# Performance work log

Hardware: AMD Instinct MI355X
Metric: run time of the kernel (lower is better)

The kernel has to match this reference:

```python
import jax, jax.numpy as jnp
import numpy as np

# Segmented linear polynomial: irreps '96x0e + 64x1o + 32x2e' -> same
MULS_IN = (96, 64, 32)   # input multiplicities per irrep segment
MULS_OUT = (96, 64, 32)  # output multiplicities per irrep segment
IRREP_DIMS = (1, 3, 5)   # 2l+1 for l = 0, 1, 2
NUM_ELEMENTS = 64        # number of indexed weight sets
BATCH = 16384            # nodes
IN_SIZE = sum(m * d for m, d in zip(MULS_IN, IRREP_DIMS))    # 448
OUT_SIZE = sum(m * d for m, d in zip(MULS_OUT, IRREP_DIMS))  # 448
W_SIZE = sum(mi * mo for mi, mo in zip(MULS_IN, MULS_OUT))   # 14336


def setup_inputs() -> dict:
    key = jax.random.key(0)
    k1, k2, k3 = jax.random.split(key, 3)
    weights = jax.random.normal(k1, (NUM_ELEMENTS, W_SIZE), dtype=jnp.float32)
    x = jax.random.normal(k2, (BATCH, IN_SIZE), dtype=jnp.float32)
    weight_indices = jax.random.randint(k3, (BATCH,), 0, NUM_ELEMENTS, dtype=jnp.int64)
    return {"weights": weights, "x": x, "weight_indices": weight_indices}


def reference(weights, x, weight_indices):
    """Indexed segmented linear: per irrep segment,
    y[b, o, m] = sum_i x[b, i, m] * W[idx[b], i, o]."""
    B = x.shape[0]
    outs = []
    w_off = 0
    x_off = 0
    for mi, mo, d in zip(MULS_IN, MULS_OUT, IRREP_DIMS):
        W_seg = weights[:, w_off:w_off + mi * mo].reshape(-1, mi, mo)  # [E, mi, mo]
        x_seg = x[:, x_off:x_off + mi * d].reshape(B, mi, d)           # [B, mi, d]
        Wg = W_seg[weight_indices]                                     # [B, mi, mo] gather
        y_seg = jnp.einsum('bim,bio->bom', x_seg, Wg)                  # [B, mo, d]
        outs.append(y_seg.reshape(B, mo * d))
        w_off += mi * mo
        x_off += mi * d
    return jnp.concatenate(outs, axis=1)  # [B, OUT_SIZE]
```

## Files before the change

### kernel.cpp

```cpp
#include <hip/hip_runtime.h>


#define BATCH     16384
#define IN_SIZE   448
#define OUT_SIZE  448
#define W_SIZE    14336
#define NELEM     64
#define RTILE     32
#define MAXTILES  576
#define WT_ELEM   15872

typedef __attribute__((ext_vector_type(8))) short short8;
typedef __attribute__((ext_vector_type(8))) unsigned short us8;
typedef __attribute__((ext_vector_type(4))) float f32x4;

__device__ __forceinline__ unsigned short f2bf(float f) {
    unsigned int u = __float_as_uint(f);
    u += 0x7fffu + ((u >> 16) & 1u);
    return (unsigned short)(u >> 16);
}


template <int MI, int MO, int SRC, int DB>
__device__ __forceinline__ void wprep_seg(const float* __restrict__ we,
                                          unsigned short* __restrict__ de,
                                          unsigned short* lw, int t) {
    constexpr int LP  = MO + 4;
    constexpr int STR = MI + 8;
    constexpr int CNT = MI * MO;
    constexpr int C8  = STR / 8;

    for (int g = t * 4; g < CNT; g += 1024) {
        const int i = g / MO, o = g - i * MO;
        const float4 v = *(const float4*)(we + SRC + g);
        ushort4 w = { f2bf(v.x), f2bf(v.y), f2bf(v.z), f2bf(v.w) };
        *(ushort4*)&lw[i * LP + o] = w;
    }
    __syncthreads();

    for (int c = t; c < MO * C8; c += 256) {
        const int o = c / C8, i0 = (c - o * C8) * 8;
        us8 w;
        #pragma unroll
        for (int k = 0; k < 8; ++k)
            w[k] = (i0 + k < MI) ? lw[(i0 + k) * LP + o] : (unsigned short)0;
        *(us8*)&de[DB + o * STR + i0] = w;
    }
}

__global__ __launch_bounds__(256) void combo_kernel(
    const int* __restrict__ widx, const float* __restrict__ weights,
    int* __restrict__ offsets, int* __restrict__ tileoff, int* __restrict__ blk2e,
    unsigned short* __restrict__ wt) {
    __shared__ __align__(16) unsigned short lw[9600];
    const int t = threadIdx.x;

    if (blockIdx.x < 192) {
        const int e = blockIdx.x / 3, seg = blockIdx.x - 3 * (blockIdx.x / 3);
        const float* __restrict__ we = weights + (size_t)e * W_SIZE;
        unsigned short* __restrict__ de = wt + (size_t)e * WT_ELEM;
        if (seg == 0)      wprep_seg<96, 96,     0,     0>(we, de, lw, t);
        else if (seg == 1) wprep_seg<64, 64,  9216,  9984>(we, de, lw, t);
        else               wprep_seg<32, 32, 13312, 14592>(we, de, lw, t);
        return;
    }

    __shared__ int h[NELEM];
    __shared__ int off_s[NELEM + 1], tl_s[NELEM + 1];
    if (t < NELEM) h[t] = 0;
    __syncthreads();
    for (int i = 0; i < 64; ++i)
        atomicAdd(&h[widx[i * 256 + t]], 1);
    __syncthreads();
    if (t == 0) {
        int o = 0, tl = 0;
        for (int e = 0; e < NELEM; ++e) {
            off_s[e] = o; tl_s[e] = tl;
            o += h[e]; tl += (h[e] + RTILE - 1) >> 5;
        }
        off_s[NELEM] = o; tl_s[NELEM] = tl;
    }
    __syncthreads();
    if (t <= NELEM) { offsets[t] = off_s[t]; tileoff[t] = tl_s[t]; }
    for (int i = t; i < MAXTILES; i += 256) blk2e[i] = -1;
    __syncthreads();
    if (t < NELEM)
        for (int bb = tl_s[t]; bb < tl_s[t + 1]; ++bb) blk2e[bb] = t;
}


template <int MI, int MO, int D, int XOFF, int YOFF, int WB>
__device__ __forceinline__ void do_seg(const float* __restrict__ x,
                                       const unsigned short* __restrict__ wt_e,
                                       const int* rid_s, int nrows,
                                       float* __restrict__ out,
                                       unsigned short* lds_w, unsigned short* lds_x,
                                       int t) {
    constexpr int XP   = MI * D + 8;
    constexpr int WSTR = MI + 8;
    constexpr int NT   = MO / 16;
    constexpr int KB   = MI / 32;
    constexpr int MTL  = 2 * D;
    constexpr int WCH  = (MO * WSTR) / 8;
    constexpr int FPT  = (MI * D) / 8;
    constexpr int NQ   = FPT / 4;
    constexpr int MOD  = MO * D;
    constexpr int NTW  = (MTL * NT) / 4;
    constexpr int F4R  = MOD / 4;

    const int r = t >> 3, j = t & 7;

    const float4* __restrict__ src =
        (const float4*)(x + (size_t)rid_s[r] * IN_SIZE + XOFF + j * FPT);
    float vv[FPT];
    #pragma unroll
    for (int q = 0; q < NQ; ++q) {
        const float4 v = src[q];
        vv[q * 4 + 0] = v.x; vv[q * 4 + 1] = v.y;
        vv[q * 4 + 2] = v.z; vv[q * 4 + 3] = v.w;
    }

    const uint4* __restrict__ wsrc = (const uint4*)(wt_e + WB);
    for (int idx = t; idx < WCH; idx += 256) ((uint4*)lds_w)[idx] = wsrc[idx];

    if (D == 1) {
        #pragma unroll
        for (int q = 0; q < NQ; ++q) {
            ushort4 w = { f2bf(vv[q * 4 + 0]), f2bf(vv[q * 4 + 1]),
                          f2bf(vv[q * 4 + 2]), f2bf(vv[q * 4 + 3]) };
            *(ushort4*)&lds_x[r * XP + j * FPT + q * 4] = w;
        }
    } else if (D == 3) {
        #pragma unroll
        for (int m = 0; m < 3; ++m) {
            us8 w;
            #pragma unroll
            for (int bq = 0; bq < 8; ++bq) w[bq] = f2bf(vv[3 * bq + m]);
            *(us8*)&lds_x[r * XP + m * MI + j * 8] = w;
        }
    } else {
        #pragma unroll
        for (int m = 0; m < 5; ++m) {
            ushort4 w = { f2bf(vv[m]), f2bf(vv[5 + m]),
                          f2bf(vv[10 + m]), f2bf(vv[15 + m]) };
            *(ushort4*)&lds_x[r * XP + m * MI + j * 4] = w;
        }
    }
    __syncthreads();

    const int lane = t & 63, w = t >> 6;
    const int row_l = lane & 15, kg = lane >> 4;
    f32x4 accs[NTW];
    #pragma unroll
    for (int q = 0; q < NTW; ++q) {
        const int ct = w + q * 4;
        const int mIdx = ct / NT, nt = ct - mIdx * NT;
        const int mt = mIdx & 1, mch = mIdx >> 1;
        f32x4 acc = {0.f, 0.f, 0.f, 0.f};
        #pragma unroll
        for (int kb = 0; kb < KB; ++kb) {
            const short8 a = *(const short8*)&lds_x[(mt * 16 + row_l) * XP + mch * MI + kb * 32 + kg * 8];
            const short8 b = *(const short8*)&lds_w[(nt * 16 + row_l) * WSTR + kb * 32 + kg * 8];
            acc = __builtin_amdgcn_mfma_f32_16x16x32_bf16(a, b, acc, 0, 0, 0);
        }
        accs[q] = acc;
    }
    __syncthreads();

    float* __restrict__ lout = (float*)lds_w;
    #pragma unroll
    for (int q = 0; q < NTW; ++q) {
        const int ct = w + q * 4;
        const int mIdx = ct / NT, nt = ct - mIdx * NT;
        const int mt = mIdx & 1, mch = mIdx >> 1;
        const int o = nt * 16 + row_l;
        #pragma unroll
        for (int jj = 0; jj < 4; ++jj) {
            const int m = mt * 16 + kg * 4 + jj;
            lout[m * MOD + o * D + mch] = accs[q][jj];
        }
    }
    __syncthreads();

    for (int idx = t; idx < RTILE * F4R; idx += 256) {
        const int rr = idx / F4R, c = idx - rr * F4R;
        if (rr < nrows) {
            float4 v = *(const float4*)&lout[rr * MOD + c * 4];
            *(float4*)&out[(size_t)rid_s[rr] * OUT_SIZE + YOFF + c * 4] = v;
        }
    }
}

__global__ __launch_bounds__(256) void gemm_kernel(
    const float* __restrict__ x, const unsigned short* __restrict__ wt,
    const int* __restrict__ widx, const int* __restrict__ offsets,
    const int* __restrict__ tileoff, const int* __restrict__ blk2e,
    float* __restrict__ out) {
    __shared__ __align__(16) unsigned short lds[13312];
    __shared__ int rid_s[RTILE];
    __shared__ int wsum[4];

    const int t   = threadIdx.x;
    const int seg = blockIdx.x / MAXTILES;
    const int tb  = blockIdx.x - seg * MAXTILES;
    const int e   = blk2e[tb];
    if (e < 0) return;
    const int tile  = tb - tileoff[e];
    const int cnt   = offsets[e + 1] - offsets[e];
    const int lo    = tile * RTILE;
    const int nrows = min(RTILE, cnt - lo);

    {
        unsigned long long m = 0;
        #pragma unroll
        for (int i = 0; i < 64; ++i)
            m |= (unsigned long long)(widx[i * 256 + t] == e) << i;
        const int c = __popcll(m);
        int xacc = c;
        #pragma unroll
        for (int d = 1; d < 64; d <<= 1) {
            const int v = __shfl_up(xacc, d, 64);
            if ((t & 63) >= d) xacc += v;
        }
        if ((t & 63) == 63) wsum[t >> 6] = xacc;
        __syncthreads();
        int wbase = 0;
        #pragma unroll
        for (int wv = 0; wv < 4; ++wv) wbase += (wv < (t >> 6)) ? wsum[wv] : 0;
        const int p = wbase + xacc - c;
        if (p < lo + RTILE && p + c > lo) {
            unsigned long long mm = m;
            int k = p;
            while (mm) {
                const int i = __ffsll((long long)mm) - 1;
                if (k >= lo) rid_s[k - lo] = i * 256 + t;
                ++k;
                if (k >= lo + RTILE) break;
                mm &= mm - 1;
            }
        }
        __syncthreads();
        if (t >= nrows && t < RTILE) rid_s[t] = rid_s[0];
        __syncthreads();
    }

    const unsigned short* wt_e = wt + (size_t)e * WT_ELEM;
    if (seg == 0)
        do_seg<96, 96, 1,   0,   0,     0>(x, wt_e, rid_s, nrows, out, lds, lds + 9984, t);
    else if (seg == 1)
        do_seg<64, 64, 3,  96,  96,  9984>(x, wt_e, rid_s, nrows, out, lds, lds + 4608, t);
    else
        do_seg<32, 32, 5, 288, 288, 14592>(x, wt_e, rid_s, nrows, out, lds, lds + 1280, t);
}


extern "C" void kernel_launch(void* const* d_in, const int* in_sizes, int n_in,
                              void* d_out, int out_size, void* d_ws, size_t ws_size,
                              hipStream_t stream) {
    const float* weights = (const float*)d_in[0];
    const float* x       = (const float*)d_in[1];
    const int*   widx    = (const int*)d_in[2];
    float*       out     = (float*)d_out;

    char* ws = (char*)d_ws;
    int* offsets = (int*)(ws + 0);
    int* tileoff = (int*)(ws + 512);
    int* blk2e   = (int*)(ws + 1024);
    unsigned short* wt = (unsigned short*)(ws + 8192);

    combo_kernel<<<193, 256, 0, stream>>>(widx, weights, offsets, tileoff, blk2e, wt);
    gemm_kernel <<<3 * MAXTILES, 256, 0, stream>>>(x, wt, widx, offsets,
                                                   tileoff, blk2e, out);
}
```

Before: 31.48 us.

## Double row tile to 64, prefetch weights early, use contiguous index scan

Raises the rows per tile from 32 to 64, so each block reuses the staged per-element weight slice across twice as many rows and fewer blocks are launched. Each thread now loads two rows of x, each wave computes twice as many MFMA tiles, and the output is written through LDS in two 32-row passes. The weight copy into LDS is moved ahead of the row-id scan so it overlaps with that scan. The index scan now reads contiguous 64-entry chunks per thread instead of strided entries. This costs more registers and LDS per block and leaves fewer blocks to spread across CUs, and partially filled 64-row tiles waste more compute.

```diff
diff --git a/kernel.cpp b/kernel.cpp
--- a/kernel.cpp
+++ b/kernel.cpp
@@ -6,8 +6,8 @@
 #define OUT_SIZE  448
 #define W_SIZE    14336
 #define NELEM     64
-#define RTILE     32
-#define MAXTILES  576
+#define RTILE     64
+#define MAXTILES  320
 #define WT_ELEM   15872
 
 typedef __attribute__((ext_vector_type(8))) short short8;
@@ -76,7 +76,7 @@
         int o = 0, tl = 0;
         for (int e = 0; e < NELEM; ++e) {
             off_s[e] = o; tl_s[e] = tl;
-            o += h[e]; tl += (h[e] + RTILE - 1) >> 5;
+            o += h[e]; tl += (h[e] + RTILE - 1) >> 6;
         }
         off_s[NELEM] = o; tl_s[NELEM] = tl;
     }
@@ -89,61 +89,65 @@
 }
 
 
-template <int MI, int MO, int D, int XOFF, int YOFF, int WB>
+template <int MI, int MO, int D, int XOFF, int YOFF, int WB, int WHALVES>
 __device__ __forceinline__ void do_seg(const float* __restrict__ x,
                                        const unsigned short* __restrict__ wt_e,
                                        const int* rid_s, int nrows,
                                        float* __restrict__ out,
-                                       unsigned short* lds_w, unsigned short* lds_x,
-                                       int t) {
+                                       unsigned short* lds, int t) {
     constexpr int XP   = MI * D + 8;
     constexpr int WSTR = MI + 8;
     constexpr int NT   = MO / 16;
     constexpr int KB   = MI / 32;
-    constexpr int MTL  = 2 * D;
-    constexpr int WCH  = (MO * WSTR) / 8;
     constexpr int FPT  = (MI * D) / 8;
     constexpr int NQ   = FPT / 4;
     constexpr int MOD  = MO * D;
-    constexpr int NTW  = (MTL * NT) / 4;
+    constexpr int NTW  = D * NT;
     constexpr int F4R  = MOD / 4;
 
+    unsigned short* lds_w = lds;
+    unsigned short* lds_x = lds + WHALVES;
+
     const int r = t >> 3, j = t & 7;
 
-    const float4* __restrict__ src =
-        (const float4*)(x + (size_t)rid_s[r] * IN_SIZE + XOFF + j * FPT);
-    float vv[FPT];
-    #pragma unroll
-    for (int q = 0; q < NQ; ++q) {
-        const float4 v = src[q];
-        vv[q * 4 + 0] = v.x; vv[q * 4 + 1] = v.y;
-        vv[q * 4 + 2] = v.z; vv[q * 4 + 3] = v.w;
-    }
-
-    const uint4* __restrict__ wsrc = (const uint4*)(wt_e + WB);
-    for (int idx = t; idx < WCH; idx += 256) ((uint4*)lds_w)[idx] = wsrc[idx];
-
-    if (D == 1) {
+    float vv[2][FPT];
+    #pragma unroll
+    for (int rr = 0; rr < 2; ++rr) {
+        const float4* __restrict__ src =
+            (const float4*)(x + (size_t)rid_s[r + rr * 32] * IN_SIZE + XOFF + j * FPT);
         #pragma unroll
         for (int q = 0; q < NQ; ++q) {
-            ushort4 w = { f2bf(vv[q * 4 + 0]), f2bf(vv[q * 4 + 1]),
-                          f2bf(vv[q * 4 + 2]), f2bf(vv[q * 4 + 3]) };
-            *(ushort4*)&lds_x[r * XP + j * FPT + q * 4] = w;
-        }
-    } else if (D == 3) {
-        #pragma unroll
-        for (int m = 0; m < 3; ++m) {
-            us8 w;
+            const float4 v = src[q];
+            vv[rr][q * 4 + 0] = v.x; vv[rr][q * 4 + 1] = v.y;
+            vv[rr][q * 4 + 2] = v.z; vv[rr][q * 4 + 3] = v.w;
+        }
+    }
+
+    #pragma unroll
+    for (int rr = 0; rr < 2; ++rr) {
+        unsigned short* __restrict__ dst = lds_x + (r + rr * 32) * XP;
+        if (D == 1) {
             #pragma unroll
-            for (int bq = 0; bq < 8; ++bq) w[bq] = f2bf(vv[3 * bq + m]);
-            *(us8*)&lds_x[r * XP + m * MI + j * 8] = w;
-        }
-    } else {
-        #pragma unroll
-        for (int m = 0; m < 5; ++m) {
-            ushort4 w = { f2bf(vv[m]), f2bf(vv[5 + m]),
-                          f2bf(vv[10 + m]), f2bf(vv[15 + m]) };
-            *(ushort4*)&lds_x[r * XP + m * MI + j * 4] = w;
+            for (int q = 0; q < NQ; ++q) {
+                ushort4 w = { f2bf(vv[rr][q * 4 + 0]), f2bf(vv[rr][q * 4 + 1]),
+                              f2bf(vv[rr][q * 4 + 2]), f2bf(vv[rr][q * 4 + 3]) };
+                *(ushort4*)&dst[j * FPT + q * 4] = w;
+            }
+        } else if (D == 3) {
+            #pragma unroll
+            for (int m = 0; m < 3; ++m) {
+                us8 w;
+                #pragma unroll
+                for (int bq = 0; bq < 8; ++bq) w[bq] = f2bf(vv[rr][3 * bq + m]);
+                *(us8*)&dst[m * MI + j * 8] = w;
+            }
+        } else {
+            #pragma unroll
+            for (int m = 0; m < 5; ++m) {
+                ushort4 w = { f2bf(vv[rr][m]), f2bf(vv[rr][5 + m]),
+                              f2bf(vv[rr][10 + m]), f2bf(vv[rr][15 + m]) };
+                *(ushort4*)&dst[m * MI + j * 4] = w;
+            }
         }
     }
     __syncthreads();
@@ -155,7 +159,7 @@
     for (int q = 0; q < NTW; ++q) {
         const int ct = w + q * 4;
         const int mIdx = ct / NT, nt = ct - mIdx * NT;
-        const int mt = mIdx & 1, mch = mIdx >> 1;
+        const int mt = mIdx & 3, mch = mIdx >> 2;
         f32x4 acc = {0.f, 0.f, 0.f, 0.f};
         #pragma unroll
         for (int kb = 0; kb < KB; ++kb) {
@@ -167,27 +171,33 @@
     }
     __syncthreads();
 
-    float* __restrict__ lout = (float*)lds_w;
-    #pragma unroll
-    for (int q = 0; q < NTW; ++q) {
-        const int ct = w + q * 4;
-        const int mIdx = ct / NT, nt = ct - mIdx * NT;
-        const int mt = mIdx & 1, mch = mIdx >> 1;
-        const int o = nt * 16 + row_l;
-        #pragma unroll
-        for (int jj = 0; jj < 4; ++jj) {
-            const int m = mt * 16 + kg * 4 + jj;
-            lout[m * MOD + o * D + mch] = accs[q][jj];
-        }
-    }
-    __syncthreads();
-
-    for (int idx = t; idx < RTILE * F4R; idx += 256) {
-        const int rr = idx / F4R, c = idx - rr * F4R;
-        if (rr < nrows) {
-            float4 v = *(const float4*)&lout[rr * MOD + c * 4];
-            *(float4*)&out[(size_t)rid_s[rr] * OUT_SIZE + YOFF + c * 4] = v;
-        }
+    float* __restrict__ lout = (float*)lds;
+    #pragma unroll
+    for (int p = 0; p < 2; ++p) {
+        #pragma unroll
+        for (int q = 0; q < NTW; ++q) {
+            const int ct = w + q * 4;
+            const int mIdx = ct / NT, nt = ct - mIdx * NT;
+            const int mt = mIdx & 3, mch = mIdx >> 2;
+            if ((mt >> 1) == p) {
+                const int o = nt * 16 + row_l;
+                #pragma unroll
+                for (int jj = 0; jj < 4; ++jj) {
+                    const int lm = (mt & 1) * 16 + kg * 4 + jj;
+                    lout[lm * MOD + o * D + mch] = accs[q][jj];
+                }
+            }
+        }
+        __syncthreads();
+        for (int idx = t; idx < 32 * F4R; idx += 256) {
+            const int rr = idx / F4R, c = idx - rr * F4R;
+            const int grow = p * 32 + rr;
+            if (grow < nrows) {
+                float4 v = *(const float4*)&lout[rr * MOD + c * 4];
+                *(float4*)&out[(size_t)rid_s[grow] * OUT_SIZE + YOFF + c * 4] = v;
+            }
+        }
+        if (p == 0) __syncthreads();
     }
 }
 
@@ -196,7 +206,7 @@
     const int* __restrict__ widx, const int* __restrict__ offsets,
     const int* __restrict__ tileoff, const int* __restrict__ blk2e,
     float* __restrict__ out) {
-    __shared__ __align__(16) unsigned short lds[13312];
+    __shared__ __align__(16) unsigned short lds[17408];
     __shared__ int rid_s[RTILE];
     __shared__ int wsum[4];
 
@@ -210,11 +220,19 @@
     const int lo    = tile * RTILE;
     const int nrows = min(RTILE, cnt - lo);
 
+    const unsigned short* wt_e = wt + (size_t)e * WT_ELEM;
+    {
+        const int WB   = (seg == 0) ? 0 : (seg == 1) ? 9984 : 14592;
+        const int WCH  = (seg == 0) ? 1248 : (seg == 1) ? 576 : 160;
+        const uint4* __restrict__ wsrc = (const uint4*)(wt_e + WB);
+        for (int idx = t; idx < WCH; idx += 256) ((uint4*)lds)[idx] = wsrc[idx];
+    }
+
     {
         unsigned long long m = 0;
         #pragma unroll
         for (int i = 0; i < 64; ++i)
-            m |= (unsigned long long)(widx[i * 256 + t] == e) << i;
+            m |= (unsigned long long)(widx[t * 64 + i] == e) << i;
         const int c = __popcll(m);
         int xacc = c;
         #pragma unroll
@@ -233,7 +251,7 @@
             int k = p;
             while (mm) {
                 const int i = __ffsll((long long)mm) - 1;
-                if (k >= lo) rid_s[k - lo] = i * 256 + t;
+                if (k >= lo) rid_s[k - lo] = t * 64 + i;
                 ++k;
                 if (k >= lo + RTILE) break;
                 mm &= mm - 1;
@@ -244,13 +262,12 @@
         __syncthreads();
     }
 
-    const unsigned short* wt_e = wt + (size_t)e * WT_ELEM;
     if (seg == 0)
-        do_seg<96, 96, 1,   0,   0,     0>(x, wt_e, rid_s, nrows, out, lds, lds + 9984, t);
+        do_seg<96, 96, 1,   0,   0,     0,  9984>(x, wt_e, rid_s, nrows, out, lds, t);
     else if (seg == 1)
-        do_seg<64, 64, 3,  96,  96,  9984>(x, wt_e, rid_s, nrows, out, lds, lds + 4608, t);
+        do_seg<64, 64, 3,  96,  96,  9984,  4608>(x, wt_e, rid_s, nrows, out, lds, t);
     else
-        do_seg<32, 32, 5, 288, 288, 14592>(x, wt_e, rid_s, nrows, out, lds, lds + 1280, t);
+        do_seg<32, 32, 5, 288, 288, 14592,  1280>(x, wt_e, rid_s, nrows, out, lds, t);
 }
 
 
```

Measured after the change: 41.80 us. +32.8%, slower.
